# Performance work log

Measured on AMD Instinct MI355X. Metric: run time of the kernel, lower is better.

The kernel has to match this reference:

```python
import jax, jax.numpy as jnp
import numpy as np

N_NODES = 50000
N_EDGES = 800000
NODE_F = 5
EDGE_F = 4
HID = 128


def _glorot(key, shape):
    fan_in, fan_out = shape[0], shape[1]
    lim = float(np.sqrt(6.0 / (fan_in + fan_out)))
    return jax.random.uniform(key, shape, jnp.float32, -lim, lim)


def setup_inputs() -> dict:
    key = jax.random.key(0)
    ks = jax.random.split(key, 12)
    x = jax.random.normal(ks[0], (N_NODES, NODE_F), jnp.float32)
    edge_attr = jax.random.normal(ks[1], (N_EDGES, EDGE_F), jnp.float32)
    edge_index = jax.random.randint(ks[2], (2, N_EDGES), 0, N_NODES, jnp.int64)
    return {
        "x": x,
        "edge_attr": edge_attr,
        "W1": _glorot(ks[3], (NODE_F, HID)),
        "b1": jnp.zeros((HID,), jnp.float32),
        "W2": _glorot(ks[4], (HID, HID)),
        "b2": jnp.zeros((HID,), jnp.float32),
        "Wm1": _glorot(ks[5], (2 * HID + EDGE_F, HID)),
        "bm1": jnp.zeros((HID,), jnp.float32),
        "Wm2": _glorot(ks[6], (HID, 1)),
        "bm2": jnp.zeros((1,), jnp.float32),
        "edge_index": edge_index,
    }


def _gcn_conv(x, W, b, row, col, norm, n_nodes):
    # GCNConv: out = D^{-1/2} (A + I) D^{-1/2} X W + b
    xw = x @ W                                   # [N, H]
    msg = norm[:, None] * xw[row]                # [E+N, H] gather + scale
    agg = jax.ops.segment_sum(msg, col, num_segments=n_nodes)
    return agg + b


def reference(x, edge_attr, W1, b1, W2, b2, Wm1, bm1, Wm2, bm2, edge_index):
    n = x.shape[0]
    src, dst = edge_index[0], edge_index[1]
    # add self-loops (PyG GCNConv default)
    loop = jnp.arange(n, dtype=edge_index.dtype)
    row = jnp.concatenate([src, loop])
    col = jnp.concatenate([dst, loop])
    # symmetric normalization, in-degree w/ self-loops
    deg = jax.ops.segment_sum(jnp.ones_like(col, dtype=x.dtype), col, num_segments=n)
    dis = jnp.where(deg > 0, jax.lax.rsqrt(deg), 0.0)
    norm = dis[row] * dis[col]

    h = jax.nn.relu(_gcn_conv(x, W1, b1, row, col, norm, n))
    h = _gcn_conv(h, W2, b2, row, col, norm, n)

    # gather-concat edge MLP
    edge_emb = jnp.concatenate([h[src], h[dst], edge_attr], axis=1)  # [E, 2H+F]
    out = jax.nn.relu(edge_emb @ Wm1 + bm1) @ Wm2 + bm2              # [E, 1]
    return jax.nn.sigmoid(out[:, 0])
```

## Files before the change

### kernel.cpp

```cpp
#include <hip/hip_runtime.h>
#include <math.h>

#define HID 128
typedef unsigned int uint;
typedef __attribute__((ext_vector_type(8))) __bf16 bf16x8;
typedef __attribute__((ext_vector_type(4))) float f32x4;
typedef __attribute__((ext_vector_type(2))) float f32x2;


__device__ __forceinline__ uint pack_bf2(float x, float y) {
    union { float f; uint u; } a, b;
    a.f = x; b.f = y;
    uint lo = (a.u + 0x7fffu + ((a.u >> 16) & 1u)) >> 16;
    uint hi = (b.u + 0x7fffu + ((b.u >> 16) & 1u)) & 0xffff0000u;
    return lo | hi;
}

__device__ __forceinline__ unsigned short bf16r(float x) {
    union { float f; uint u; } a; a.f = x;
    return (unsigned short)((a.u + 0x7fffu + ((a.u >> 16) & 1u)) >> 16);
}

__device__ __forceinline__ f32x2 bf2f(uint v) {
    union { uint u[2]; f32x2 f; } r;
    r.u[0] = v << 16;
    r.u[1] = v & 0xffff0000u;
    return r.f;
}

__device__ __forceinline__ f32x2 mk2(float s) { f32x2 r; r.x = s; r.y = s; return r; }
__device__ __forceinline__ f32x2 max2z(f32x2 a) {
    f32x2 r; r.x = fmaxf(a.x, 0.f); r.y = fmaxf(a.y, 0.f); return r;
}
__device__ __forceinline__ f32x2 shfl_xor2(f32x2 v, int m) {
    f32x2 r; r.x = __shfl_xor(v.x, m, 64); r.y = __shfl_xor(v.y, m, 64); return r;
}


__global__ void zero_prep(int* __restrict__ cnt, int N,
                          const float* __restrict__ W2, const float* __restrict__ Wm1,
                          const float* __restrict__ b2, const float* __restrict__ bm1,
                          uint* __restrict__ fWc, float* __restrict__ brow) {
    int stride = gridDim.x * blockDim.x;
    int t0 = blockIdx.x * blockDim.x + threadIdx.x;
    for (int i = t0; i < N; i += stride) cnt[i] = 0;
    for (int i = t0; i < 16384; i += stride) {
        int p = i & 3, lane = (i >> 2) & 63, kk = (i >> 8) & 3, ct = i >> 10;
        int k = kk * 32 + (lane >> 4) * 8 + p * 2;
        int n2 = ct * 16 + (lane & 15);
        const float* wmc = (n2 < 128) ? (Wm1 + n2) : (Wm1 + 128 * HID + (n2 - 128));
        const float* w2r0 = W2 + (size_t)k * HID;
        const float* w2r1 = w2r0 + HID;
        float d0 = 0.f, d1 = 0.f;
        for (int j = 0; j < HID; ++j) {
            float wm = wmc[(size_t)j * HID];
            d0 += w2r0[j] * wm;
            d1 += w2r1[j] * wm;
        }
        fWc[i] = pack_bf2(d0, d1);
    }
    for (int i = t0; i < 256; i += stride) {
        const float* wmc = (i < 128) ? (Wm1 + i) : (Wm1 + 128 * HID + (i - 128));
        float d = 0.f;
        for (int j = 0; j < HID; ++j) d += b2[j] * wmc[(size_t)j * HID];
        brow[i] = d + ((i < 128) ? bm1[i] : 0.f);
    }
}

__global__ void hist_rank(const int* __restrict__ dst, int* __restrict__ cnt,
                          int* __restrict__ rank, int E) {
    int e = blockIdx.x * blockDim.x + threadIdx.x;
    if (e < E) rank[e] = atomicAdd(&cnt[dst[e]], 1);
}

__global__ void scan1(const int* __restrict__ cnt, int* __restrict__ excl,
                      int* __restrict__ bsum, int N) {
    __shared__ int sh[256];
    int tid = threadIdx.x;
    int gid = blockIdx.x * 256 + tid;
    int v = (gid < N) ? cnt[gid] : 0;
    sh[tid] = v;
    __syncthreads();
    for (int o = 1; o < 256; o <<= 1) {
        int t = (tid >= o) ? sh[tid - o] : 0;
        __syncthreads();
        sh[tid] += t;
        __syncthreads();
    }
    if (gid < N) excl[gid] = sh[tid] - v;
    if (tid == 255) bsum[blockIdx.x] = sh[255];
}

__global__ void scan3x(const int* __restrict__ cnt, int* __restrict__ rowptr,
                       const int* __restrict__ bsum,
                       float* __restrict__ dis, const float* __restrict__ x,
                       float* __restrict__ xps, int N, int E, int NB) {
    __shared__ int sh[256];
    __shared__ int ex[256];
    int tid = threadIdx.x;
    int v = (tid < NB) ? bsum[tid] : 0;
    sh[tid] = v;
    __syncthreads();
    for (int o = 1; o < 256; o <<= 1) {
        int t = (tid >= o) ? sh[tid - o] : 0;
        __syncthreads();
        sh[tid] += t;
        __syncthreads();
    }
    ex[tid] = sh[tid] - v;
    __syncthreads();
    int gid = blockIdx.x * 256 + tid;
    if (gid < N) {
        rowptr[gid] = rowptr[gid] + ex[blockIdx.x];
        float dn = rsqrtf((float)cnt[gid] + 1.0f);
        dis[gid] = dn;
        const float* xr = x + (size_t)gid * 5;
        float* xo = xps + (size_t)gid * 8;
        *(float4*)xo = make_float4(dn * xr[0], dn * xr[1], dn * xr[2], dn * xr[3]);
        xo[4] = dn * xr[4];
    }
    if (gid == N) rowptr[N] = E;
}

__global__ void scatter2(const int* __restrict__ src, const int* __restrict__ dst,
                         const int* __restrict__ rowptr, const int* __restrict__ rank,
                         uint2* __restrict__ csr2, int E) {
    int e = blockIdx.x * blockDim.x + threadIdx.x;
    if (e < E) {
        int d = dst[e];
        int pos = rowptr[d] + rank[e];
        csr2[pos] = make_uint2((uint)src[e] | ((uint)d << 16), (uint)e);
    }
}

__launch_bounds__(256)
__global__ void layer1_kernel(const float* __restrict__ xps, const uint2* __restrict__ csr2,
                              const int* __restrict__ rowptr, const float* __restrict__ dis,
                              const float* __restrict__ W1, const float* __restrict__ b1,
                              uint* __restrict__ hs1, int N) {
    __shared__ float sW[5 * HID];
    __shared__ float sb[HID];
    int tid = threadIdx.x;
    for (int i = tid; i < 5 * HID; i += 256) sW[i] = W1[i];
    for (int i = tid; i < HID; i += 256) sb[i] = b1[i];
    __syncthreads();

    int n = blockIdx.x * 256 + tid;
    if (n >= N) return;
    int beg = rowptr[n], end = rowptr[n + 1];
    float a0 = 0.f, a1 = 0.f, a2 = 0.f, a3 = 0.f, a4 = 0.f;
    for (int i = beg; i < end; ++i) {
        int s = (int)(csr2[i].x & 0xffffu);
        float4 v = *(const float4*)(xps + (size_t)s * 8);
        float v4 = xps[(size_t)s * 8 + 4];
        a0 += v.x; a1 += v.y; a2 += v.z; a3 += v.w; a4 += v4;
    }
    {
        float4 v = *(const float4*)(xps + (size_t)n * 8);
        float v4 = xps[(size_t)n * 8 + 4];
        a0 += v.x; a1 += v.y; a2 += v.z; a3 += v.w; a4 += v4;
    }
    float dn = dis[n];
    a0 *= dn; a1 *= dn; a2 *= dn; a3 *= dn; a4 *= dn;

    uint* op = hs1 + (size_t)n * 64;
    #pragma unroll 4
    for (int p = 0; p < 64; ++p) {
        int j = p * 2;
        float t0 = sb[j]     + a0 * sW[j]     + a1 * sW[HID + j]     + a2 * sW[2*HID + j]
                             + a3 * sW[3*HID + j] + a4 * sW[4*HID + j];
        float t1 = sb[j + 1] + a0 * sW[j + 1] + a1 * sW[HID + j + 1] + a2 * sW[2*HID + j + 1]
                             + a3 * sW[3*HID + j + 1] + a4 * sW[4*HID + j + 1];
        op[p] = pack_bf2(fmaxf(t0, 0.f) * dn, fmaxf(t1, 0.f) * dn);
    }
}

__launch_bounds__(256)
__global__ void agg_gemm(const uint4* __restrict__ hs1, const uint2* __restrict__ csr2,
                         const int* __restrict__ rowptr, const float* __restrict__ dis,
                         const uint4* __restrict__ Bf, const float* __restrict__ brow,
                         unsigned short* __restrict__ out, int N) {
    __shared__ uint gt[16][64];
    int wave = threadIdx.x >> 6, lane = threadIdx.x & 63;
    int gl = lane & 15, grp = lane >> 4;
    int nb = blockIdx.x * 16;

    for (int q = 0; q < 4; ++q) {
        int r = wave * 4 + q;
        int n = nb + r;
        if (n < N) {
            int beg = rowptr[n], end = rowptr[n + 1];
            f32x2 acc[4];
            #pragma unroll
            for (int p = 0; p < 4; ++p) acc[p] = mk2(0.f);
            for (int base = beg + grp; base < end; base += 16) {
                int i1 = base + 4, i2 = base + 8, i3 = base + 12;
                int s0 = (int)(csr2[base].x & 0xffffu);
                int s1 = (int)(csr2[(i1 < end) ? i1 : beg].x & 0xffffu);
                int s2 = (int)(csr2[(i2 < end) ? i2 : beg].x & 0xffffu);
                int s3 = (int)(csr2[(i3 < end) ? i3 : beg].x & 0xffffu);
                uint4 v0 = hs1[(size_t)s0 * 16 + gl];
                uint4 v1 = hs1[(size_t)s1 * 16 + gl];
                uint4 v2 = hs1[(size_t)s2 * 16 + gl];
                uint4 v3 = hs1[(size_t)s3 * 16 + gl];
                f32x2 w1 = mk2((i1 < end) ? 1.f : 0.f);
                f32x2 w2 = mk2((i2 < end) ? 1.f : 0.f);
                f32x2 w3 = mk2((i3 < end) ? 1.f : 0.f);
                acc[0] += bf2f(v0.x);  acc[1] += bf2f(v0.y);
                acc[2] += bf2f(v0.z);  acc[3] += bf2f(v0.w);
                acc[0] += bf2f(v1.x) * w1;  acc[1] += bf2f(v1.y) * w1;
                acc[2] += bf2f(v1.z) * w1;  acc[3] += bf2f(v1.w) * w1;
                acc[0] += bf2f(v2.x) * w2;  acc[1] += bf2f(v2.y) * w2;
                acc[2] += bf2f(v2.z) * w2;  acc[3] += bf2f(v2.w) * w2;
                acc[0] += bf2f(v3.x) * w3;  acc[1] += bf2f(v3.y) * w3;
                acc[2] += bf2f(v3.z) * w3;  acc[3] += bf2f(v3.w) * w3;
            }
            #pragma unroll
            for (int p = 0; p < 4; ++p) {
                acc[p] += shfl_xor2(acc[p], 16);
                acc[p] += shfl_xor2(acc[p], 32);
            }
            if (grp == 0) {
                uint4 sv = hs1[(size_t)n * 16 + gl];
                f32x2 dn = mk2(dis[n]);
                f32x2 o0 = (acc[0] + bf2f(sv.x)) * dn;
                f32x2 o1 = (acc[1] + bf2f(sv.y)) * dn;
                f32x2 o2 = (acc[2] + bf2f(sv.z)) * dn;
                f32x2 o3 = (acc[3] + bf2f(sv.w)) * dn;
                gt[r][gl * 4]     = pack_bf2(o0.x, o0.y);
                gt[r][gl * 4 + 1] = pack_bf2(o1.x, o1.y);
                gt[r][gl * 4 + 2] = pack_bf2(o2.x, o2.y);
                gt[r][gl * 4 + 3] = pack_bf2(o3.x, o3.y);
            }
        } else if (grp == 0) {
            gt[r][gl * 4] = 0; gt[r][gl * 4 + 1] = 0;
            gt[r][gl * 4 + 2] = 0; gt[r][gl * 4 + 3] = 0;
        }
    }
    __syncthreads();

    int quad = lane >> 4;
    bf16x8 afr[4];
    #pragma unroll
    for (int kk = 0; kk < 4; ++kk)
        afr[kk] = *(const bf16x8*)&gt[gl][kk * 16 + quad * 4];

    for (int cc = 0; cc < 4; ++cc) {
        int c = wave * 4 + cc;
        f32x4 acc = {0.f, 0.f, 0.f, 0.f};
        #pragma unroll
        for (int kk = 0; kk < 4; ++kk) {
            bf16x8 bfr = *(const bf16x8*)&Bf[(size_t)(c * 4 + kk) * 64 + lane];
            acc = __builtin_amdgcn_mfma_f32_16x16x32_bf16(afr[kk], bfr, acc, 0, 0, 0);
        }
        float bv = brow[c * 16 + gl];
        #pragma unroll
        for (int reg = 0; reg < 4; ++reg) {
            int row = nb + quad * 4 + reg;
            if (row < N)
                out[(size_t)row * 256 + c * 16 + gl] = bf16r(acc[reg] + bv);
        }
    }
}

__launch_bounds__(256)
__global__ void edge_mlp_kernel(const uint4* __restrict__ HsHd, const float4* __restrict__ ea,
                                const uint2* __restrict__ csr2,
                                const float* __restrict__ Wb, const float* __restrict__ Wm2,
                                const float* __restrict__ bm2,
                                float* __restrict__ out, int E) {
    int lane = threadIdx.x & 63;
    int gl = lane & 15, grp = lane >> 4;

    f32x2 wb[4][4], w2[4];
    #pragma unroll
    for (int k = 0; k < 4; ++k) {
        const f32x2* wp = (const f32x2*)(Wb + k * HID + gl * 8);
        #pragma unroll
        for (int p = 0; p < 4; ++p) wb[k][p] = wp[p];
    }
    {
        const f32x2* wp = (const f32x2*)(Wm2 + gl * 8);
        #pragma unroll
        for (int p = 0; p < 4; ++p) w2[p] = wp[p];
    }
    float b2v = bm2[0];

    int gwave = (blockIdx.x * blockDim.x + threadIdx.x) >> 6;
    int nw = (gridDim.x * blockDim.x) >> 6;
    for (int base = gwave * 16; base < E; base += nw * 16) {
        int i0 = base + grp * 4;
        uint2 ce[4];
        uint4 hv[4], dv[4];
        float4 eav[4];
        #pragma unroll
        for (int t = 0; t < 4; ++t) {
            int i = i0 + t;
            int j = (i < E) ? i : (E - 1);
            ce[t] = csr2[j];
            hv[t] = HsHd[(size_t)(ce[t].x & 0xffffu) * 32 + gl];
            dv[t] = HsHd[(size_t)(ce[t].x >> 16) * 32 + 16 + gl];
            eav[t] = ea[ce[t].y];
        }
        float pr[4];
        #pragma unroll
        for (int t = 0; t < 4; ++t) {
            uint hu[4] = {hv[t].x, hv[t].y, hv[t].z, hv[t].w};
            uint du[4] = {dv[t].x, dv[t].y, dv[t].z, dv[t].w};
            f32x2 e0 = mk2(eav[t].x), e1 = mk2(eav[t].y);
            f32x2 e2 = mk2(eav[t].z), e3 = mk2(eav[t].w);
            f32x2 p2 = mk2(0.f);
            #pragma unroll
            for (int p = 0; p < 4; ++p) {
                f32x2 tt = bf2f(hu[p]) + bf2f(du[p]);
                tt += e0 * wb[0][p];
                tt += e1 * wb[1][p];
                tt += e2 * wb[2][p];
                tt += e3 * wb[3][p];
                tt = max2z(tt);
                p2 += tt * w2[p];
            }
            pr[t] = p2.x + p2.y;
        }
        #pragma unroll
        for (int o = 1; o <= 8; o <<= 1) {
            #pragma unroll
            for (int t = 0; t < 4; ++t) pr[t] += __shfl_xor(pr[t], o, 64);
        }
        if (gl == 0) {
            #pragma unroll
            for (int t = 0; t < 4; ++t) {
                int i = i0 + t;
                if (i < E) out[ce[t].y] = 1.f / (1.f + expf(-(pr[t] + b2v)));
            }
        }
    }
}


extern "C" void kernel_launch(void* const* d_in, const int* in_sizes, int n_in,
                              void* d_out, int out_size, void* d_ws, size_t ws_size,
                              hipStream_t stream) {
    const float* x    = (const float*)d_in[0];
    const float* ea   = (const float*)d_in[1];
    const float* W1   = (const float*)d_in[2];
    const float* b1   = (const float*)d_in[3];
    const float* W2   = (const float*)d_in[4];
    const float* b2   = (const float*)d_in[5];
    const float* Wm1  = (const float*)d_in[6];
    const float* bm1  = (const float*)d_in[7];
    const float* Wm2  = (const float*)d_in[8];
    const float* bm2  = (const float*)d_in[9];
    const int*   ei   = (const int*)d_in[10];

    const int N = in_sizes[0] / 5;
    const int E = in_sizes[1] / 4;
    const int* src = ei;
    const int* dst = ei + E;
    float* out = (float*)d_out;

    char* ws = (char*)d_ws;
    size_t off = 0;
    auto alloc = [&](size_t bytes) -> void* {
        void* p = ws + off;
        off = (off + bytes + 255) & ~(size_t)255;
        return p;
    };
    int*    cnt    = (int*)alloc((size_t)N * 4);
    int*    rowptr = (int*)alloc((size_t)(N + 1) * 4);
    int*    bsum   = (int*)alloc(256 * 4);
    float*  dis    = (float*)alloc((size_t)N * 4);
    int*    rank   = (int*)alloc((size_t)(E + 8) * 4);
    uint2*  csr2   = (uint2*)alloc((size_t)(E + 8) * 8);
    float*  xps    = (float*)alloc((size_t)N * 8 * 4);
    uint*   hs1    = (uint*)alloc((size_t)N * 64 * 4);
    uint*   HsHd   = (uint*)alloc((size_t)N * 128 * 4);
    uint*   fWc    = (uint*)alloc(16384 * 4);
    float*  brow   = (float*)alloc(256 * 4);
    (void)ws_size; (void)n_in; (void)out_size;

    const int NB = (N + 255) / 256;
    const int EB = (E + 255) / 256;

    zero_prep<<<NB, 256, 0, stream>>>(cnt, N, W2, Wm1, b2, bm1, fWc, brow);
    hist_rank<<<EB, 256, 0, stream>>>(dst, cnt, rank, E);
    scan1<<<NB, 256, 0, stream>>>(cnt, rowptr, bsum, N);
    scan3x<<<NB, 256, 0, stream>>>(cnt, rowptr, bsum, dis, x, xps, N, E, NB);
    scatter2<<<EB, 256, 0, stream>>>(src, dst, rowptr, rank, csr2, E);

    layer1_kernel<<<NB, 256, 0, stream>>>(xps, csr2, rowptr, dis, W1, b1, hs1, N);

    agg_gemm<<<(N + 15) / 16, 256, 0, stream>>>((const uint4*)hs1, csr2, rowptr, dis,
                                                (const uint4*)fWc, brow,
                                                (unsigned short*)HsHd, N);

    edge_mlp_kernel<<<2048, 256, 0, stream>>>((const uint4*)HsHd, (const float4*)ea, csr2,
                                              Wm1 + 256 * HID, Wm2, bm2, out, E);
}
```

Before: 265.4 us.

## Pack scaled node features to bf16, chunk edge MLP contiguously, split zero/prep

Stores the degree-scaled input features as packed bf16 in a 16-byte record instead of 32 bytes of fp32, halving the gather traffic in layer 1 at some precision cost. The edge MLP now gives each wave a contiguous chunk of CSR edges, with the block index swizzled across groups of eight, instead of a grid-stride loop, aiming for better locality of destination-node rows. The count zeroing moves to hipMemsetAsync and the weight-folding prep runs on a small 65-block grid. The sigmoid uses exp2f instead of expf.

```diff
diff --git a/kernel.cpp b/kernel.cpp
--- a/kernel.cpp
+++ b/kernel.cpp
@@ -37,14 +37,12 @@
 }
 
 
-__global__ void zero_prep(int* __restrict__ cnt, int N,
-                          const float* __restrict__ W2, const float* __restrict__ Wm1,
-                          const float* __restrict__ b2, const float* __restrict__ bm1,
-                          uint* __restrict__ fWc, float* __restrict__ brow) {
-    int stride = gridDim.x * blockDim.x;
+__global__ void prep_kernel(const float* __restrict__ W2, const float* __restrict__ Wm1,
+                            const float* __restrict__ b2, const float* __restrict__ bm1,
+                            uint* __restrict__ fWc, float* __restrict__ brow) {
     int t0 = blockIdx.x * blockDim.x + threadIdx.x;
-    for (int i = t0; i < N; i += stride) cnt[i] = 0;
-    for (int i = t0; i < 16384; i += stride) {
+    if (t0 < 16384) {
+        int i = t0;
         int p = i & 3, lane = (i >> 2) & 63, kk = (i >> 8) & 3, ct = i >> 10;
         int k = kk * 32 + (lane >> 4) * 8 + p * 2;
         int n2 = ct * 16 + (lane & 15);
@@ -58,8 +56,8 @@
             d1 += w2r1[j] * wm;
         }
         fWc[i] = pack_bf2(d0, d1);
-    }
-    for (int i = t0; i < 256; i += stride) {
+    } else if (t0 < 16384 + 256) {
+        int i = t0 - 16384;
         const float* wmc = (i < 128) ? (Wm1 + i) : (Wm1 + 128 * HID + (i - 128));
         float d = 0.f;
         for (int j = 0; j < HID; ++j) d += b2[j] * wmc[(size_t)j * HID];
@@ -94,7 +92,7 @@
 __global__ void scan3x(const int* __restrict__ cnt, int* __restrict__ rowptr,
                        const int* __restrict__ bsum,
                        float* __restrict__ dis, const float* __restrict__ x,
-                       float* __restrict__ xps, int N, int E, int NB) {
+                       uint4* __restrict__ xps, int N, int E, int NB) {
     __shared__ int sh[256];
     __shared__ int ex[256];
     int tid = threadIdx.x;
@@ -115,9 +113,12 @@
         float dn = rsqrtf((float)cnt[gid] + 1.0f);
         dis[gid] = dn;
         const float* xr = x + (size_t)gid * 5;
-        float* xo = xps + (size_t)gid * 8;
-        *(float4*)xo = make_float4(dn * xr[0], dn * xr[1], dn * xr[2], dn * xr[3]);
-        xo[4] = dn * xr[4];
+        uint4 pk;
+        pk.x = pack_bf2(dn * xr[0], dn * xr[1]);
+        pk.y = pack_bf2(dn * xr[2], dn * xr[3]);
+        pk.z = pack_bf2(dn * xr[4], 0.f);
+        pk.w = 0u;
+        xps[gid] = pk;
     }
     if (gid == N) rowptr[N] = E;
 }
@@ -134,7 +135,7 @@
 }
 
 __launch_bounds__(256)
-__global__ void layer1_kernel(const float* __restrict__ xps, const uint2* __restrict__ csr2,
+__global__ void layer1_kernel(const uint4* __restrict__ xps, const uint2* __restrict__ csr2,
                               const int* __restrict__ rowptr, const float* __restrict__ dis,
                               const float* __restrict__ W1, const float* __restrict__ b1,
                               uint* __restrict__ hs1, int N) {
@@ -151,14 +152,14 @@
     float a0 = 0.f, a1 = 0.f, a2 = 0.f, a3 = 0.f, a4 = 0.f;
     for (int i = beg; i < end; ++i) {
         int s = (int)(csr2[i].x & 0xffffu);
-        float4 v = *(const float4*)(xps + (size_t)s * 8);
-        float v4 = xps[(size_t)s * 8 + 4];
-        a0 += v.x; a1 += v.y; a2 += v.z; a3 += v.w; a4 += v4;
+        uint4 v = xps[s];
+        f32x2 v01 = bf2f(v.x), v23 = bf2f(v.y), v4 = bf2f(v.z);
+        a0 += v01.x; a1 += v01.y; a2 += v23.x; a3 += v23.y; a4 += v4.x;
     }
     {
-        float4 v = *(const float4*)(xps + (size_t)n * 8);
-        float v4 = xps[(size_t)n * 8 + 4];
-        a0 += v.x; a1 += v.y; a2 += v.z; a3 += v.w; a4 += v4;
+        uint4 v = xps[n];
+        f32x2 v01 = bf2f(v.x), v23 = bf2f(v.y), v4 = bf2f(v.z);
+        a0 += v01.x; a1 += v01.y; a2 += v23.x; a3 += v23.y; a4 += v4.x;
     }
     float dn = dis[n];
     a0 *= dn; a1 *= dn; a2 *= dn; a3 *= dn; a4 *= dn;
@@ -270,6 +271,7 @@
                                 const float* __restrict__ bm2,
                                 float* __restrict__ out, int E) {
     int lane = threadIdx.x & 63;
+    int wave = threadIdx.x >> 6;
     int gl = lane & 15, grp = lane >> 4;
 
     f32x2 wb[4][4], w2[4];
@@ -286,9 +288,17 @@
     }
     float b2v = bm2[0];
 
-    int gwave = (blockIdx.x * blockDim.x + threadIdx.x) >> 6;
-    int nw = (gridDim.x * blockDim.x) >> 6;
-    for (int base = gwave * 16; base < E; base += nw * 16) {
+    int nb = gridDim.x;
+    int lb = (blockIdx.x & 7) * (nb >> 3) + (blockIdx.x >> 3);
+    int lw = lb * (blockDim.x >> 6) + wave;
+    int nw = (nb * blockDim.x) >> 6;
+    long chunk = (((long)E + (long)nw * 16 - 1) / ((long)nw * 16)) * 16;
+    long s64 = (long)lw * chunk;
+    int start = (s64 < E) ? (int)s64 : E;
+    long e64 = s64 + chunk;
+    int stop = (e64 < E) ? (int)e64 : E;
+
+    for (int base = start; base < stop; base += 16) {
         int i0 = base + grp * 4;
         uint2 ce[4];
         uint4 hv[4], dv[4];
@@ -331,7 +341,8 @@
             #pragma unroll
             for (int t = 0; t < 4; ++t) {
                 int i = i0 + t;
-                if (i < E) out[ce[t].y] = 1.f / (1.f + expf(-(pr[t] + b2v)));
+                if (i < E)
+                    out[ce[t].y] = 1.f / (1.f + exp2f(-1.44269504f * (pr[t] + b2v)));
             }
         }
     }
@@ -372,7 +383,7 @@
     float*  dis    = (float*)alloc((size_t)N * 4);
     int*    rank   = (int*)alloc((size_t)(E + 8) * 4);
     uint2*  csr2   = (uint2*)alloc((size_t)(E + 8) * 8);
-    float*  xps    = (float*)alloc((size_t)N * 8 * 4);
+    uint4*  xps    = (uint4*)alloc((size_t)N * 16);
     uint*   hs1    = (uint*)alloc((size_t)N * 64 * 4);
     uint*   HsHd   = (uint*)alloc((size_t)N * 128 * 4);
     uint*   fWc    = (uint*)alloc(16384 * 4);
@@ -382,7 +393,8 @@
     const int NB = (N + 255) / 256;
     const int EB = (E + 255) / 256;
 
-    zero_prep<<<NB, 256, 0, stream>>>(cnt, N, W2, Wm1, b2, bm1, fWc, brow);
+    hipMemsetAsync(cnt, 0, (size_t)N * 4, stream);
+    prep_kernel<<<65, 256, 0, stream>>>(W2, Wm1, b2, bm1, fWc, brow);
     hist_rank<<<EB, 256, 0, stream>>>(dst, cnt, rank, E);
     scan1<<<NB, 256, 0, stream>>>(cnt, rowptr, bsum, N);
     scan3x<<<NB, 256, 0, stream>>>(cnt, rowptr, bsum, dis, x, xps, N, E, NB);
```

Result: no change. 270.2 us (+1.8%).
